# Kernel tuning notes

Hardware: AMD Instinct MI355X
Metric: run time of the kernel (lower is better)

Reference implementation:

```python
import jax, jax.numpy as jnp
import numpy as np

H = 20   # num heads
D = 64   # head dim (hidden_size=1280)
N_IMG = 4
N_LBL = 4
SCALE_IMG = 1.0
SCALE_LBL = 1.0


def setup_inputs() -> dict:
    key = jax.random.key(0)
    ks = jax.random.split(key, 12)
    B, S, C, Dc = 4, 4096, 1280, 2048
    L = 77 + N_IMG + N_LBL  # 85 encoder tokens
    w = lambda k, shp: jax.random.normal(k, shp, dtype=jnp.float32) * 0.02
    return {
        "hidden_states": jax.random.normal(ks[0], (B, S, C), dtype=jnp.float32),
        "encoder_hidden_states": jax.random.normal(ks[1], (B, L, Dc), dtype=jnp.float32),
        "Wq": w(ks[2], (C, C)),
        "Wk": w(ks[3], (Dc, C)),
        "Wv": w(ks[4], (Dc, C)),
        "Wk_ip": w(ks[5], (Dc, C)),
        "Wv_ip": w(ks[6], (Dc, C)),
        "Wk_lbl": w(ks[7], (Dc, C)),
        "Wv_lbl": w(ks[8], (Dc, C)),
        "Wo": w(ks[9], (C, C)),
        "bo": jnp.zeros((C,), dtype=jnp.float32),
    }


def _attend(q, enc, Wk_, Wv_):
    # q: [B, S, H, D]; enc: [B, L, Dc]
    B, L = enc.shape[0], enc.shape[1]
    k = (enc @ Wk_).reshape(B, L, H, D)
    v = (enc @ Wv_).reshape(B, L, H, D)
    scores = jnp.einsum("bqhd,bkhd->bhqk", q, k) * (D ** -0.5)
    p = jax.nn.softmax(scores, axis=-1)
    return jnp.einsum("bhqk,bkhd->bqhd", p, v)


def reference(hidden_states, encoder_hidden_states, Wq, Wk, Wv,
              Wk_ip, Wv_ip, Wk_lbl, Wv_lbl, Wo, bo):
    B, S, C = hidden_states.shape
    end = encoder_hidden_states.shape[1] - N_IMG - N_LBL
    enc_text = encoder_hidden_states[:, :end]
    enc_img = encoder_hidden_states[:, end:end + N_IMG]
    enc_lbl = encoder_hidden_states[:, end + N_IMG:]

    q = (hidden_states @ Wq).reshape(B, S, H, D)

    out = _attend(q, enc_text, Wk, Wv)
    out = out + SCALE_IMG * _attend(q, enc_img, Wk_ip, Wv_ip)
    out = out + SCALE_LBL * _attend(q, enc_lbl, Wk_lbl, Wv_lbl)

    out = out.reshape(B, S, C) @ Wo + bo
    return out + hidden_states  # residual_connection=True, rescale=1.0
```

## Files before the change

kernel.cpp:

```cpp
#include <hip/hip_runtime.h>
#include <hip/hip_bf16.h>

typedef unsigned short u16;
using f32x4  = __attribute__((ext_vector_type(4))) float;
using bf16x8 = __attribute__((ext_vector_type(8))) short;

#define N_B 4
#define N_S 4096
#define N_C 1280
#define N_DC 2048
#define N_H 20
#define N_D 64

__device__ __forceinline__ u16 f2b(float f) {
  union { float f; unsigned u; } x; x.f = f;
  return (u16)((x.u + 0x7fffu + ((x.u >> 16) & 1u)) >> 16);
}

__device__ __forceinline__ void gld16(const u16* g, u16* l) {
  __builtin_amdgcn_global_load_lds(
      (const __attribute__((address_space(1))) unsigned int*)(g),
      (__attribute__((address_space(3))) unsigned int*)(l), 16, 0, 0);
}

__global__ void k_cvt(const float* __restrict__ src, u16* __restrict__ dst, int n8) {
  for (int i = blockIdx.x * 256 + threadIdx.x; i < n8; i += gridDim.x * 256) {
    const float4 v0 = *(const float4*)(src + (size_t)i * 8);
    const float4 v1 = *(const float4*)(src + (size_t)i * 8 + 4);
    alignas(16) u16 t[8];
    t[0] = f2b(v0.x); t[1] = f2b(v0.y); t[2] = f2b(v0.z); t[3] = f2b(v0.w);
    t[4] = f2b(v1.x); t[5] = f2b(v1.y); t[6] = f2b(v1.z); t[7] = f2b(v1.w);
    *(uint4*)(dst + (size_t)i * 8) = *(uint4*)t;
  }
}

struct TPargs { const float* s[8]; u16* d[8]; int K[8]; };

__global__ void k_transpose8(TPargs a) {
  int z = blockIdx.z;
  const float* __restrict__ src = a.s[z];
  u16* __restrict__ dst = a.d[z];
  int K = a.K[z];
  int k0 = blockIdx.y * 32;
  if (k0 >= K) return;
  __shared__ float tl[32][33];
  int n0 = blockIdx.x * 32;
  int tx = threadIdx.x, ty = threadIdx.y;
#pragma unroll
  for (int j = 0; j < 32; j += 8)
    tl[ty + j][tx] = src[(size_t)(k0 + ty + j) * N_C + (n0 + tx)];
  __syncthreads();
#pragma unroll
  for (int j = 0; j < 32; j += 8)
    dst[(size_t)(n0 + ty + j) * K + (k0 + tx)] = f2b(tl[tx][ty + j]);
}

__global__ void k_encpack(const float* __restrict__ enc, u16* __restrict__ txt,
                          u16* __restrict__ img, u16* __restrict__ lbl) {
  int row = blockIdx.x;
  int b = row / 85, l = row % 85;
  const float* s = enc + (size_t)row * N_DC;
  u16* d;
  if (l < 77)      d = txt + (size_t)(b * 77 + l) * N_DC;
  else if (l < 81) d = img + (size_t)(b * 4 + (l - 77)) * N_DC;
  else             d = lbl + (size_t)(b * 4 + (l - 81)) * N_DC;
  for (int i = threadIdx.x; i < N_DC; i += 256) d[i] = f2b(s[i]);
}


__device__ __forceinline__ void stage64(const u16* __restrict__ g, int ldK,
                                        int row0, int kk, u16* ldsb,
                                        int w, int lane) {
  int r = w * 8 + (lane >> 3);
  int gslot = ((lane & 7) ^ (lane >> 3)) << 3;
  gld16(g + (size_t)(row0 + r) * ldK + kk + gslot, ldsb + w * 512);
}
__device__ __forceinline__ void stageA4(const u16* Ag, int K, int kk, u16* ldsb,
                                        int w, int lane) {
#pragma unroll
  for (int j = 0; j < 4; j++)
    stage64(Ag, K, j * 64, kk, ldsb + j * 4096, w, lane);
}
__device__ __forceinline__ void stageB5(const u16* Bg, int K, int kk, u16* ldsb,
                                        int w, int lane) {
#pragma unroll
  for (int j = 0; j < 5; j++)
    stage64(Bg, K, j * 64, kk, ldsb + j * 4096, w, lane);
}

#define RD_A2(aoff, mh)                                                      \
  _Pragma("unroll") for (int mi = 0; mi < 2; mi++) {                         \
    _Pragma("unroll") for (int ks = 0; ks < 2; ks++) {                       \
      int row = wr * 128 + ((mh) * 2 + mi) * 16 + lrow;                      \
      int slot = (ks * 4 + g) ^ (lane & 7);                                  \
      af[mi][ks] = *(const bf16x8*)&lds[(aoff) + row * 64 + slot * 8];       \
    }                                                                        \
  }

#define RD_B5(boff)                                                          \
  _Pragma("unroll") for (int n = 0; n < 5; n++) {                            \
    _Pragma("unroll") for (int ks = 0; ks < 2; ks++) {                       \
      int row = wc * 80 + n * 16 + lrow;                                     \
      int slot = (ks * 4 + g) ^ (lane & 7);                                  \
      bf[n][ks] = *(const bf16x8*)&lds[(boff) + row * 64 + slot * 8];        \
    }                                                                        \
  }

#define MFMA20(mh)                                                           \
  _Pragma("unroll") for (int ks = 0; ks < 2; ks++) {                         \
    _Pragma("unroll") for (int mi = 0; mi < 2; mi++) {                       \
      _Pragma("unroll") for (int n = 0; n < 5; n++)                          \
        acc[(mh) * 2 + mi][n] = __builtin_amdgcn_mfma_f32_16x16x32_bf16(     \
            af[mi][ks], bf[n][ks], acc[(mh) * 2 + mi][n], 0, 0, 0);          \
    }                                                                        \
  }

#define BARR()  __builtin_amdgcn_s_barrier()
#define VM0()   asm volatile("s_waitcnt vmcnt(0)" ::: "memory")
#define PRIO(x) __builtin_amdgcn_s_setprio(x)

template<int EPI>
__global__ __launch_bounds__(512, 1)
void gemm8p(const u16* __restrict__ A, const u16* __restrict__ Bt,
            void* __restrict__ Cv, int M, int N, int K, float scale,
            const float* __restrict__ bias, const float* __restrict__ resid) {
  __shared__ __align__(16) u16 lds[73728];
  const int t = threadIdx.x, lane = t & 63, w = t >> 6;
  const int wr = w >> 2, wc = w & 3;
  const int lrow = lane & 15, g = lane >> 4;

  int nt = N / 320;
  int nwg = gridDim.x, bid = blockIdx.x;
  int swz = ((nwg & 7) == 0) ? ((bid & 7) * (nwg >> 3) + (bid >> 3)) : bid;
  int bm = swz / nt, bn = swz % nt;

  const u16* Ag = A  + (size_t)bm * 256 * K;
  const u16* Bg = Bt + (size_t)bn * 320 * K;
  const int NT = K >> 6;

  f32x4 acc[8][5] = {};
  bf16x8 af[2][2], bf[5][2];

  stageA4(Ag, K, 0, lds + 0,     w, lane);
  stageB5(Bg, K, 0, lds + 32768, w, lane);
  VM0();
  BARR();

  for (int tt = 0; tt < NT; ++tt) {
    int c = tt & 1;
    int aof  = c * 16384,        bof  = 32768 + c * 20480;
    int aof1 = (c ^ 1) * 16384,  bof1 = 32768 + (c ^ 1) * 20480;
    if (tt + 1 < NT) {
      stageA4(Ag, K, (tt + 1) * 64, lds + aof1, w, lane);
      stageB5(Bg, K, (tt + 1) * 64, lds + bof1, w, lane);
    }
    RD_A2(aof, 0); RD_B5(bof);
    PRIO(1); MFMA20(0); PRIO(0);
    RD_A2(aof, 1);
    PRIO(1); MFMA20(1); PRIO(0);
    RD_A2(aof, 2);
    PRIO(1); MFMA20(2); PRIO(0);
    RD_A2(aof, 3);
    PRIO(1); MFMA20(3); PRIO(0);
    VM0();
    BARR();
  }

#pragma unroll
  for (int m = 0; m < 8; m++) {
    int row = bm * 256 + wr * 128 + m * 16 + g * 4;
#pragma unroll
    for (int n = 0; n < 5; n++) {
      int col = bn * 320 + wc * 80 + n * 16 + lrow;
#pragma unroll
      for (int j = 0; j < 4; j++) {
        float v = acc[m][n][j];
        if constexpr (EPI == 1)
          ((u16*)Cv)[(size_t)(row + j) * N + col] = f2b(v * scale);
        else
          ((float*)Cv)[(size_t)(row + j) * N + col] =
              v + bias[col] + resid[(size_t)(row + j) * N + col];
      }
    }
  }
}

__global__ __launch_bounds__(256, 2)
void kv_gemm(const u16* __restrict__ etxt, const u16* __restrict__ eimg, const u16* __restrict__ elbl,
             const u16* __restrict__ wk,   const u16* __restrict__ wv,
             const u16* __restrict__ wkip, const u16* __restrict__ wvip,
             const u16* __restrict__ wklb, const u16* __restrict__ wvlb,
             u16* ktxt, u16* vtxt, u16* kimg, u16* vimg, u16* klbl, u16* vlbl) {
  __shared__ __align__(16) u16 lds[2][2][8192];
  int bn = blockIdx.x, my = blockIdx.y, kv = blockIdx.z;
  const u16 *A, *Bt; u16* C; int M, bm;
  if (my < 3)       { A = etxt; M = 308; bm = my; Bt = kv ? wv   : wk;   C = kv ? vtxt : ktxt; }
  else if (my == 3) { A = eimg; M = 16;  bm = 0;  Bt = kv ? wvip : wkip; C = kv ? vimg : kimg; }
  else              { A = elbl; M = 16;  bm = 0;  Bt = kv ? wvlb : wklb; C = kv ? vlbl : klbl; }
  const int K = 2048;
  int t = threadIdx.x, lane = t & 63, w = t >> 6;
  int wm = w >> 1, wn = w & 1;
  int c8 = lane & 7, rsub = lane >> 3;

  f32x4 acc[4][4] = {};

#define KVSTAGE(kt, buf)                                                      \
  {                                                                           \
    int k0 = (kt) * 64;                                                       \
    _Pragma("unroll") for (int i2 = 0; i2 < 4; i2++) {                        \
      int rloc = w * 32 + i2 * 8;                                             \
      int ra = bm * 128 + rloc + rsub; if (ra >= M) ra = M - 1;               \
      int rb = bn * 128 + rloc + rsub;                                        \
      gld16(A  + (size_t)ra * K + k0 + c8 * 8, &lds[buf][0][rloc * 64]);      \
      gld16(Bt + (size_t)rb * K + k0 + c8 * 8, &lds[buf][1][rloc * 64]);      \
    }                                                                         \
  }

  KVSTAGE(0, 0);
  asm volatile("s_waitcnt vmcnt(0)" ::: "memory");
  __syncthreads();
  int cur = 0;
  for (int kt = 0; kt < 32; kt++) {
    if (kt < 31) KVSTAGE(kt + 1, cur ^ 1);
#pragma unroll
    for (int ks = 0; ks < 2; ks++) {
      bf16x8 afr[4], bfr[4];
#pragma unroll
      for (int m = 0; m < 4; m++)
        afr[m] = *(bf16x8*)&lds[cur][0][(wm * 64 + m * 16 + (lane & 15)) * 64 + ks * 32 + (lane >> 4) * 8];
#pragma unroll
      for (int n = 0; n < 4; n++)
        bfr[n] = *(bf16x8*)&lds[cur][1][(wn * 64 + n * 16 + (lane & 15)) * 64 + ks * 32 + (lane >> 4) * 8];
#pragma unroll
      for (int m = 0; m < 4; m++)
#pragma unroll
        for (int n = 0; n < 4; n++)
          acc[m][n] = __builtin_amdgcn_mfma_f32_16x16x32_bf16(afr[m], bfr[n], acc[m][n], 0, 0, 0);
    }
    asm volatile("s_waitcnt vmcnt(0)" ::: "memory");
    __syncthreads();
    cur ^= 1;
  }
#undef KVSTAGE

#pragma unroll
  for (int m = 0; m < 4; m++) {
    int row = bm * 128 + wm * 64 + m * 16 + ((lane >> 4) << 2);
#pragma unroll
    for (int n = 0; n < 4; n++) {
      int col = bn * 128 + wn * 64 + n * 16 + (lane & 15);
#pragma unroll
      for (int j = 0; j < 4; j++) {
        int r = row + j;
        if (r >= M) continue;
        ((u16*)C)[(size_t)r * 1280 + col] = f2b(acc[m][n][j]);
      }
    }
  }
}

#define QSTR 72
#define PSTR 104

__global__ __launch_bounds__(256, 2)
void attn_kern(const u16* __restrict__ q,
               const u16* __restrict__ ktxt, const u16* __restrict__ vtxt,
               const u16* __restrict__ kimg, const u16* __restrict__ vimg,
               const u16* __restrict__ klbl, const u16* __restrict__ vlbl,
               u16* __restrict__ outa) {
  __shared__ __align__(16) char smem[45568];
  u16* Qs = (u16*)smem;
  u16* Ks = (u16*)(smem + 18432);
  u16* Ps = (u16*)smem;
  u16* Vt = (u16*)(smem + 32256);

  int st = blockIdx.x, h = blockIdx.y, b = blockIdx.z;
  int t = threadIdx.x, lane = t & 63, w = t >> 6;
  int s0 = st * 128;
  int c = lane & 15, g = lane >> 4;

  for (int i = t; i < 27136 / 16; i += 256)
    ((uint4*)(smem + 18432))[i] = make_uint4(0, 0, 0, 0);
#pragma unroll
  for (int i = 0; i < 4; i++) {
    int cid = t + i * 256; int r = cid >> 3, c8 = cid & 7;
    *(uint4*)&Qs[r * QSTR + c8 * 8] =
        *(const uint4*)(q + (size_t)(b * N_S + s0 + r) * N_C + h * N_D + c8 * 8);
  }
  __syncthreads();
  for (int cid = t; cid < 680; cid += 256) {
    int l = cid >> 3, c8 = cid & 7;
    const u16* p;
    if (l < 77)      p = ktxt + (size_t)(b * 77 + l) * N_C + h * N_D + c8 * 8;
    else if (l < 81) p = kimg + (size_t)(b * 4 + l - 77) * N_C + h * N_D + c8 * 8;
    else             p = klbl + (size_t)(b * 4 + l - 81) * N_C + h * N_D + c8 * 8;
    int row = (l < 77) ? l : l + 3;
    *(uint4*)&Ks[row * QSTR + c8 * 8] = *(const uint4*)p;
  }
  for (int e = t; e < 85 * 64; e += 256) {
    int l = e >> 6, d = e & 63;
    const u16* p;
    if (l < 77)      p = vtxt + (size_t)(b * 77 + l) * N_C + h * N_D + d;
    else if (l < 81) p = vimg + (size_t)(b * 4 + l - 77) * N_C + h * N_D + d;
    else             p = vlbl + (size_t)(b * 4 + l - 81) * N_C + h * N_D + d;
    int slot = (l < 77) ? l : l + 3;
    Vt[d * PSTR + slot] = *p;
  }
  __syncthreads();

  f32x4 sacc[2][6] = {};
#pragma unroll
  for (int ks = 0; ks < 2; ks++) {
    bf16x8 aq[2], bk[6];
#pragma unroll
    for (int m = 0; m < 2; m++)
      aq[m] = *(bf16x8*)&Qs[(w * 32 + m * 16 + c) * QSTR + ks * 32 + g * 8];
#pragma unroll
    for (int n = 0; n < 6; n++)
      bk[n] = *(bf16x8*)&Ks[(n * 16 + c) * QSTR + ks * 32 + g * 8];
#pragma unroll
    for (int m = 0; m < 2; m++)
#pragma unroll
      for (int n = 0; n < 6; n++)
        sacc[m][n] = __builtin_amdgcn_mfma_f32_16x16x32_bf16(aq[m], bk[n], sacc[m][n], 0, 0, 0);
  }
  __syncthreads();

  const float NEG = -1e30f;
#pragma unroll
  for (int m = 0; m < 2; m++) {
#pragma unroll
    for (int j = 0; j < 4; j++) {
      float tmax = NEG;
#pragma unroll
      for (int n = 0; n < 5; n++)
        if (n * 16 + c < 77) tmax = fmaxf(tmax, sacc[m][n][j]);
#pragma unroll
      for (int off = 1; off < 16; off <<= 1) tmax = fmaxf(tmax, __shfl_xor(tmax, off));
      float pv[5], tsum = 0.f;
#pragma unroll
      for (int n = 0; n < 5; n++) {
        float v = (n * 16 + c < 77) ? __expf(sacc[m][n][j] - tmax) : 0.f;
        pv[n] = v; tsum += v;
      }
#pragma unroll
      for (int off = 1; off < 16; off <<= 1) tsum += __shfl_xor(tsum, off);
      float v5 = sacc[m][5][j];
      float imax = (c < 4) ? v5 : NEG;
#pragma unroll
      for (int off = 1; off < 16; off <<= 1) imax = fmaxf(imax, __shfl_xor(imax, off));
      float ie = (c < 4) ? __expf(v5 - imax) : 0.f, isum = ie;
#pragma unroll
      for (int off = 1; off < 16; off <<= 1) isum += __shfl_xor(isum, off);
      float lmax = (c >= 4 && c < 8) ? v5 : NEG;
#pragma unroll
      for (int off = 1; off < 16; off <<= 1) lmax = fmaxf(lmax, __shfl_xor(lmax, off));
      float le = (c >= 4 && c < 8) ? __expf(v5 - lmax) : 0.f, lsum = le;
#pragma unroll
      for (int off = 1; off < 16; off <<= 1) lsum += __shfl_xor(lsum, off);

      float rt = 1.f / tsum;
      float p5 = (c < 4) ? ie / isum : ((c < 8) ? le / lsum : 0.f);
      int rowl = w * 32 + m * 16 + g * 4 + j;
#pragma unroll
      for (int n = 0; n < 5; n++)
        Ps[rowl * PSTR + n * 16 + c] = f2b(pv[n] * rt);
      Ps[rowl * PSTR + 80 + c] = f2b(p5);
    }
  }
  __syncthreads();

  f32x4 oacc[2][4] = {};
#pragma unroll
  for (int ks = 0; ks < 3; ks++) {
    bf16x8 ap[2], bv[4];
#pragma unroll
    for (int m = 0; m < 2; m++)
      ap[m] = *(bf16x8*)&Ps[(w * 32 + m * 16 + c) * PSTR + ks * 32 + g * 8];
#pragma unroll
    for (int n = 0; n < 4; n++)
      bv[n] = *(bf16x8*)&Vt[(n * 16 + c) * PSTR + ks * 32 + g * 8];
#pragma unroll
    for (int m = 0; m < 2; m++)
#pragma unroll
      for (int n = 0; n < 4; n++)
        oacc[m][n] = __builtin_amdgcn_mfma_f32_16x16x32_bf16(ap[m], bv[n], oacc[m][n], 0, 0, 0);
  }

#pragma unroll
  for (int m = 0; m < 2; m++) {
    int rbase = w * 32 + m * 16 + g * 4;
#pragma unroll
    for (int n = 0; n < 4; n++) {
      int d = n * 16 + c;
#pragma unroll
      for (int j = 0; j < 4; j++) {
        int s = s0 + rbase + j;
        outa[(size_t)(b * N_S + s) * N_C + h * N_D + d] = f2b(oacc[m][n][j]);
      }
    }
  }
}

extern "C" void kernel_launch(void* const* d_in, const int* in_sizes, int n_in,
                              void* d_out, int out_size, void* d_ws, size_t ws_size,
                              hipStream_t stream) {
  const float* hs   = (const float*)d_in[0];
  const float* enc  = (const float*)d_in[1];
  const float* Wq   = (const float*)d_in[2];
  const float* Wk   = (const float*)d_in[3];
  const float* Wv   = (const float*)d_in[4];
  const float* Wkip = (const float*)d_in[5];
  const float* Wvip = (const float*)d_in[6];
  const float* Wklb = (const float*)d_in[7];
  const float* Wvlb = (const float*)d_in[8];
  const float* Wo   = (const float*)d_in[9];
  const float* bo   = (const float*)d_in[10];

  if (ws_size < 83087360u) return;
  char* ws = (char*)d_ws;
  u16* wq_t   = (u16*)(ws + 0);
  u16* wo_t   = (u16*)(ws + 3276800);
  u16* wk_t   = (u16*)(ws + 6553600);
  u16* wv_t   = (u16*)(ws + 11796480);
  u16* wkip_t = (u16*)(ws + 17039360);
  u16* wvip_t = (u16*)(ws + 22282240);
  u16* wklb_t = (u16*)(ws + 27525120);
  u16* wvlb_t = (u16*)(ws + 32768000);
  u16* etxt   = (u16*)(ws + 38010880);
  u16* eimg   = (u16*)(ws + 39272448);
  u16* elbl   = (u16*)(ws + 39337984);
  u16* ktxt   = (u16*)(ws + 39403520);
  u16* vtxt   = (u16*)(ws + 40192000);
  u16* kimg   = (u16*)(ws + 40980480);
  u16* vimg   = (u16*)(ws + 41021440);
  u16* klbl   = (u16*)(ws + 41062400);
  u16* vlbl   = (u16*)(ws + 41103360);
  u16* attn   = (u16*)(ws + 41144320);
  u16* qbuf   = (u16*)d_out;
  u16* hsb    = (u16*)d_out + (size_t)N_S * N_B * N_C;

  k_cvt<<<2048, 256, 0, stream>>>(hs, hsb, (N_B * N_S * N_C) / 8);

  TPargs tp;
  tp.s[0] = Wq;   tp.d[0] = wq_t;   tp.K[0] = 1280;
  tp.s[1] = Wo;   tp.d[1] = wo_t;   tp.K[1] = 1280;
  tp.s[2] = Wk;   tp.d[2] = wk_t;   tp.K[2] = 2048;
  tp.s[3] = Wv;   tp.d[3] = wv_t;   tp.K[3] = 2048;
  tp.s[4] = Wkip; tp.d[4] = wkip_t; tp.K[4] = 2048;
  tp.s[5] = Wvip; tp.d[5] = wvip_t; tp.K[5] = 2048;
  tp.s[6] = Wklb; tp.d[6] = wklb_t; tp.K[6] = 2048;
  tp.s[7] = Wvlb; tp.d[7] = wvlb_t; tp.K[7] = 2048;
  k_transpose8<<<dim3(40, 64, 8), dim3(32, 8), 0, stream>>>(tp);

  k_encpack<<<340, 256, 0, stream>>>(enc, etxt, eimg, elbl);

  gemm8p<1><<<256, 512, 0, stream>>>(hsb, wq_t, qbuf, 16384, 1280, 1280,
                                     0.125f, nullptr, nullptr);
  kv_gemm<<<dim3(10, 5, 2), 256, 0, stream>>>(etxt, eimg, elbl,
                                              wk_t, wv_t, wkip_t, wvip_t, wklb_t, wvlb_t,
                                              ktxt, vtxt, kimg, vimg, klbl, vlbl);

  attn_kern<<<dim3(32, N_H, N_B), 256, 0, stream>>>(qbuf, ktxt, vtxt, kimg, vimg,
                                                    klbl, vlbl, attn);
  gemm8p<2><<<256, 512, 0, stream>>>(attn, wo_t, d_out, 16384, 1280, 1280,
                                     1.f, bo, hs);
}
```

Baseline: 257.2 us.

## Shrink GEMM tiles to 128x160 with 4 waves and 2 blocks per CU

```diff
diff --git a/kernel.cpp b/kernel.cpp
--- a/kernel.cpp
+++ b/kernel.cpp
@@ -68,30 +68,30 @@
 }
 
 
-__device__ __forceinline__ void stage64(const u16* __restrict__ g, int ldK,
+__device__ __forceinline__ void stage32(const u16* __restrict__ g, int ldK,
                                         int row0, int kk, u16* ldsb,
                                         int w, int lane) {
-  int r = w * 8 + (lane >> 3);
+  int r = row0 + w * 8 + (lane >> 3);
   int gslot = ((lane & 7) ^ (lane >> 3)) << 3;
-  gld16(g + (size_t)(row0 + r) * ldK + kk + gslot, ldsb + w * 512);
-}
-__device__ __forceinline__ void stageA4(const u16* Ag, int K, int kk, u16* ldsb,
-                                        int w, int lane) {
+  gld16(g + (size_t)r * ldK + kk + gslot, ldsb + w * 512);
+}
+__device__ __forceinline__ void stageA(const u16* Ag, int K, int kk, u16* ldsb,
+                                       int w, int lane) {
 #pragma unroll
   for (int j = 0; j < 4; j++)
-    stage64(Ag, K, j * 64, kk, ldsb + j * 4096, w, lane);
-}
-__device__ __forceinline__ void stageB5(const u16* Bg, int K, int kk, u16* ldsb,
-                                        int w, int lane) {
+    stage32(Ag, K, j * 32, kk, ldsb + j * 2048, w, lane);
+}
+__device__ __forceinline__ void stageB(const u16* Bg, int K, int kk, u16* ldsb,
+                                       int w, int lane) {
 #pragma unroll
   for (int j = 0; j < 5; j++)
-    stage64(Bg, K, j * 64, kk, ldsb + j * 4096, w, lane);
+    stage32(Bg, K, j * 32, kk, ldsb + j * 2048, w, lane);
 }
 
 #define RD_A2(aoff, mh)                                                      \
   _Pragma("unroll") for (int mi = 0; mi < 2; mi++) {                         \
     _Pragma("unroll") for (int ks = 0; ks < 2; ks++) {                       \
-      int row = wr * 128 + ((mh) * 2 + mi) * 16 + lrow;                      \
+      int row = wr * 64 + ((mh) * 2 + mi) * 16 + lrow;                       \
       int slot = (ks * 4 + g) ^ (lane & 7);                                  \
       af[mi][ks] = *(const bf16x8*)&lds[(aoff) + row * 64 + slot * 8];       \
     }                                                                        \
@@ -106,13 +106,11 @@
     }                                                                        \
   }
 
-#define MFMA20(mh)                                                           \
+#define MFMA10(mh)                                                           \
   _Pragma("unroll") for (int ks = 0; ks < 2; ks++) {                         \
-    _Pragma("unroll") for (int mi = 0; mi < 2; mi++) {                       \
-      _Pragma("unroll") for (int n = 0; n < 5; n++)                          \
-        acc[(mh) * 2 + mi][n] = __builtin_amdgcn_mfma_f32_16x16x32_bf16(     \
-            af[mi][ks], bf[n][ks], acc[(mh) * 2 + mi][n], 0, 0, 0);          \
-    }                                                                        \
+    _Pragma("unroll") for (int n = 0; n < 5; n++)                            \
+      acc[mh][n] = __builtin_amdgcn_mfma_f32_16x16x32_bf16(                  \
+          af[(mh) & 1][ks], bf[n][ks], acc[mh][n], 0, 0, 0);                 \
   }
 
 #define BARR()  __builtin_amdgcn_s_barrier()
@@ -120,58 +118,55 @@
 #define PRIO(x) __builtin_amdgcn_s_setprio(x)
 
 template<int EPI>
-__global__ __launch_bounds__(512, 1)
+__global__ __launch_bounds__(256, 2)
 void gemm8p(const u16* __restrict__ A, const u16* __restrict__ Bt,
             void* __restrict__ Cv, int M, int N, int K, float scale,
             const float* __restrict__ bias, const float* __restrict__ resid) {
-  __shared__ __align__(16) u16 lds[73728];
+  __shared__ __align__(16) u16 lds[36864];
   const int t = threadIdx.x, lane = t & 63, w = t >> 6;
-  const int wr = w >> 2, wc = w & 3;
+  const int wr = w >> 1, wc = w & 1;
   const int lrow = lane & 15, g = lane >> 4;
 
-  int nt = N / 320;
+  int nt = N / 160;
   int nwg = gridDim.x, bid = blockIdx.x;
   int swz = ((nwg & 7) == 0) ? ((bid & 7) * (nwg >> 3) + (bid >> 3)) : bid;
   int bm = swz / nt, bn = swz % nt;
 
-  const u16* Ag = A  + (size_t)bm * 256 * K;
-  const u16* Bg = Bt + (size_t)bn * 320 * K;
+  const u16* Ag = A  + (size_t)bm * 128 * K;
+  const u16* Bg = Bt + (size_t)bn * 160 * K;
   const int NT = K >> 6;
 
-  f32x4 acc[8][5] = {};
+  f32x4 acc[4][5] = {};
   bf16x8 af[2][2], bf[5][2];
 
-  stageA4(Ag, K, 0, lds + 0,     w, lane);
-  stageB5(Bg, K, 0, lds + 32768, w, lane);
+  stageA(Ag, K, 0, lds + 0,     w, lane);
+  stageB(Bg, K, 0, lds + 16384, w, lane);
   VM0();
   BARR();
 
   for (int tt = 0; tt < NT; ++tt) {
     int c = tt & 1;
-    int aof  = c * 16384,        bof  = 32768 + c * 20480;
-    int aof1 = (c ^ 1) * 16384,  bof1 = 32768 + (c ^ 1) * 20480;
+    int aof  = c * 8192,        bof  = 16384 + c * 10240;
+    int aof1 = (c ^ 1) * 8192,  bof1 = 16384 + (c ^ 1) * 10240;
     if (tt + 1 < NT) {
-      stageA4(Ag, K, (tt + 1) * 64, lds + aof1, w, lane);
-      stageB5(Bg, K, (tt + 1) * 64, lds + bof1, w, lane);
-    }
-    RD_A2(aof, 0); RD_B5(bof);
-    PRIO(1); MFMA20(0); PRIO(0);
+      stageA(Ag, K, (tt + 1) * 64, lds + aof1, w, lane);
+      stageB(Bg, K, (tt + 1) * 64, lds + bof1, w, lane);
+    }
+    RD_B5(bof);
+    RD_A2(aof, 0);
+    PRIO(1); MFMA10(0); MFMA10(1); PRIO(0);
     RD_A2(aof, 1);
-    PRIO(1); MFMA20(1); PRIO(0);
-    RD_A2(aof, 2);
-    PRIO(1); MFMA20(2); PRIO(0);
-    RD_A2(aof, 3);
-    PRIO(1); MFMA20(3); PRIO(0);
+    PRIO(1); MFMA10(2); MFMA10(3); PRIO(0);
     VM0();
     BARR();
   }
 
 #pragma unroll
-  for (int m = 0; m < 8; m++) {
-    int row = bm * 256 + wr * 128 + m * 16 + g * 4;
+  for (int m = 0; m < 4; m++) {
+    int row = bm * 128 + wr * 64 + m * 16 + g * 4;
 #pragma unroll
     for (int n = 0; n < 5; n++) {
-      int col = bn * 320 + wc * 80 + n * 16 + lrow;
+      int col = bn * 160 + wc * 80 + n * 16 + lrow;
 #pragma unroll
       for (int j = 0; j < 4; j++) {
         float v = acc[m][n][j];
@@ -455,14 +450,14 @@
 
   k_encpack<<<340, 256, 0, stream>>>(enc, etxt, eimg, elbl);
 
-  gemm8p<1><<<256, 512, 0, stream>>>(hsb, wq_t, qbuf, 16384, 1280, 1280,
-                                     0.125f, nullptr, nullptr);
+  gemm8p<1><<<1024, 256, 0, stream>>>(hsb, wq_t, qbuf, 16384, 1280, 1280,
+                                      0.125f, nullptr, nullptr);
   kv_gemm<<<dim3(10, 5, 2), 256, 0, stream>>>(etxt, eimg, elbl,
                                               wk_t, wv_t, wkip_t, wvip_t, wklb_t, wvlb_t,
                                               ktxt, vtxt, kimg, vimg, klbl, vlbl);
 
   attn_kern<<<dim3(32, N_H, N_B), 256, 0, stream>>>(qbuf, ktxt, vtxt, kimg, vimg,
                                                     klbl, vlbl, attn);
-  gemm8p<2><<<256, 512, 0, stream>>>(attn, wo_t, d_out, 16384, 1280, 1280,
-                                     1.f, bo, hs);
-}
+  gemm8p<2><<<1024, 256, 0, stream>>>(attn, wo_t, d_out, 16384, 1280, 1280,
+                                      1.f, bo, hs);
+}
```

Result: no change. 260.5 us (+1.3%).
